# Performance work log

Measured on AMD Instinct MI355X. Metric: run time of the kernel, lower is better.

Reference implementation:

```python
import jax, jax.numpy as jnp
import numpy as np

N = 100000        # num nodes
F_IN = 256        # params['topo_feature']
C = 128           # params['num_edge'] (hidden & GCN channels)
E = 1_600_000     # num edges (avg degree 16)


def setup_inputs() -> dict:
    key = jax.random.key(0)
    k = jax.random.split(key, 6)
    x = jax.random.normal(k[0], (N, F_IN), dtype=jnp.float32)
    edge_index = jax.random.randint(k[1], (2, E), 0, N, dtype=jnp.int32)
    # fc1: Linear(F_IN, C)
    W1 = jax.random.normal(k[2], (C, F_IN), dtype=jnp.float32) * (1.0 / np.sqrt(F_IN))
    b1 = jnp.zeros((C,), dtype=jnp.float32)
    # GCNConv linear: Linear(C, C, bias=False) weight + separate bias added post-aggregation
    W2 = jax.random.normal(k[3], (C, C), dtype=jnp.float32) * (1.0 / np.sqrt(C))
    b2 = jnp.zeros((C,), dtype=jnp.float32)
    return {"x": x, "edge_index": edge_index, "W1": W1, "b1": b1, "W2": W2, "b2": b2}


def reference(x, edge_index, W1, b1, W2, b2):
    # fc1 + relu
    h = jax.nn.relu(x @ W1.T + b1)                       # [N, C]
    # GCNConv: transform, add self-loops, sym-normalize, scatter-add
    z = h @ W2.T                                         # [N, C]
    loop = jnp.arange(N, dtype=edge_index.dtype)
    src = jnp.concatenate([edge_index[0], loop])         # [E+N]
    dst = jnp.concatenate([edge_index[1], loop])         # [E+N]
    deg = jax.ops.segment_sum(jnp.ones_like(dst, jnp.float32), dst, num_segments=N)
    dinv = jnp.where(deg > 0, jax.lax.rsqrt(jnp.maximum(deg, 1.0)), 0.0)
    norm = (dinv[src] * dinv[dst])[:, None]              # [E+N, 1]
    out = jax.ops.segment_sum(z[src] * norm, dst, num_segments=N) + b2
    return out
```

## Files before the change

### kernel.cpp

```cpp
#include <hip/hip_runtime.h>

typedef unsigned short ushort;
typedef __bf16 bf16x8 __attribute__((ext_vector_type(8)));
typedef float f32x4 __attribute__((ext_vector_type(4)));

#define F_IN 256
#define CCH  128
#define BSH  7
#define BNODES 128
#define NBUCK 1024
#define CHUNK 8192

#define LDA 40
#define LDH 136

__device__ __forceinline__ ushort f2bf(float f) {
    union { float f; unsigned i; } u; u.f = f;
    unsigned r = u.i + 0x7fffu + ((u.i >> 16) & 1u);
    return (ushort)(r >> 16);
}
__device__ __forceinline__ float2 bf2f2(unsigned u) {
    union { unsigned i; float f; } lo, hi;
    lo.i = u << 16;
    hi.i = u & 0xffff0000u;
    return make_float2(lo.f, hi.f);
}

__global__ __launch_bounds__(256)
void hist_cvt(const int* __restrict__ dst, int* __restrict__ hist2D, int E, int nchunks,
              const float* __restrict__ W1, const float* __restrict__ W2,
              ushort* __restrict__ w1b, ushort* __restrict__ w2b)
{
    const int blk = blockIdx.x, t = threadIdx.x;
    if (blk >= nchunks) {
        int i = (blk - nchunks) * 256 + t;
        if (i < CCH * F_IN) w1b[i] = f2bf(W1[i]);
        else {
            int j = i - CCH * F_IN;
            if (j < CCH * CCH) w2b[j] = f2bf(W2[j]);
        }
        return;
    }
    __shared__ int h[NBUCK];
    for (int i = t; i < NBUCK; i += 256) h[i] = 0;
    __syncthreads();
    int cb = blk * CHUNK, ce = min(cb + CHUNK, E);
    for (int e = cb + t; e < ce; e += 256)
        atomicAdd(&h[dst[e] >> BSH], 1);
    __syncthreads();
    for (int i = t; i < NBUCK; i += 256)
        hist2D[blk * NBUCK + i] = h[i];
}

__global__ __launch_bounds__(1024)
void scan2d(const int* __restrict__ hist2D, int* __restrict__ pref2D,
            int* __restrict__ base, int nchunks)
{
    __shared__ int s[NBUCK];
    const int t = threadIdx.x;
    int run = 0;
#pragma unroll 4
    for (int c = 0; c < nchunks; c++) {
        int v = hist2D[c * NBUCK + t];
        pref2D[c * NBUCK + t] = run;
        run += v;
    }
    s[t] = run;
    __syncthreads();
    for (int off = 1; off < NBUCK; off <<= 1) {
        int x = (t >= off) ? s[t - off] : 0;
        __syncthreads();
        s[t] += x;
        __syncthreads();
    }
    base[t] = s[t] - run;
    if (t == NBUCK - 1) base[NBUCK] = s[t];
}

__global__ __launch_bounds__(256)
void partition_kernel(const int* __restrict__ src, const int* __restrict__ dst,
                      const int* __restrict__ hist2D, const int* __restrict__ pref2D,
                      const int* __restrict__ base, unsigned* __restrict__ pairs, int E)
{
    __shared__ int lbase[NBUCK];
    __shared__ int lcur[NBUCK];
    __shared__ int rb2[NBUCK];
    __shared__ int ssum[256];
    __shared__ unsigned sp[CHUNK];
    __shared__ ushort  sb[CHUNK];
    const int t = threadIdx.x, blk = blockIdx.x;

    int4 cv = *(const int4*)&hist2D[blk * NBUCK + 4 * t];
    int tsum = cv.x + cv.y + cv.z + cv.w;
    ssum[t] = tsum;
    __syncthreads();
    for (int off = 1; off < 256; off <<= 1) {
        int x = (t >= off) ? ssum[t - off] : 0;
        __syncthreads();
        ssum[t] += x;
        __syncthreads();
    }
    int texcl = ssum[t] - tsum;
    lbase[4 * t]     = texcl;
    lbase[4 * t + 1] = texcl + cv.x;
    lbase[4 * t + 2] = texcl + cv.x + cv.y;
    lbase[4 * t + 3] = texcl + cv.x + cv.y + cv.z;
    lcur[4 * t]     = lbase[4 * t];
    lcur[4 * t + 1] = lbase[4 * t + 1];
    lcur[4 * t + 2] = lbase[4 * t + 2];
    lcur[4 * t + 3] = lbase[4 * t + 3];
    for (int i = t; i < NBUCK; i += 256)
        rb2[i] = base[i] + pref2D[blk * NBUCK + i];
    __syncthreads();

    const int cb = blk * CHUNK, ce = min(cb + CHUNK, E);
    for (int e = cb + t; e < ce; e += 256) {
        int d = dst[e];
        int b = d >> BSH;
        unsigned packed = ((unsigned)src[e] << BSH) | (unsigned)(d & (BNODES - 1));
        int p = atomicAdd(&lcur[b], 1);
        sp[p] = packed;
        sb[p] = (ushort)b;
    }
    __syncthreads();
    const int cnt = ce - cb;
    for (int i = t; i < cnt; i += 256) {
        int b = sb[i];
        pairs[rb2[b] + (i - lbase[b])] = sp[i];
    }
}

__global__ __launch_bounds__(256)
void bucket_csr(const unsigned* __restrict__ pairs, const int* __restrict__ base,
                int* __restrict__ row_start, float* __restrict__ dinv,
                unsigned* __restrict__ csr, int N, int E)
{
    __shared__ int deg[BNODES];
    __shared__ int s[BNODES];
    __shared__ int cur[BNODES];
    const int b = blockIdx.x, t = threadIdx.x;
    if (t < BNODES) deg[t] = 0;
    __syncthreads();
    const int rb = base[b], re = base[b + 1];
    for (int e = rb + t; e < re; e += 256)
        atomicAdd(&deg[pairs[e] & (BNODES - 1)], 1);
    __syncthreads();
    int v = (t < BNODES) ? deg[t] : 0;
    if (t < BNODES) s[t] = v;
    __syncthreads();
    for (int off = 1; off < BNODES; off <<= 1) {
        int x = (t >= off && t < BNODES) ? s[t - off] : 0;
        __syncthreads();
        if (t < BNODES) s[t] += x;
        __syncthreads();
    }
    const int n0 = b << BSH;
    if (t < BNODES) {
        int excl = s[t] - v;
        cur[t] = excl;
        if (n0 + t < N) {
            row_start[n0 + t] = rb + excl;
            dinv[n0 + t] = rsqrtf((float)v + 1.0f);
        }
    }
    if (b == gridDim.x - 1 && t == 0) row_start[N] = E;
    __syncthreads();
    for (int e = rb + t; e < re; e += 256) {
        unsigned p = pairs[e];
        int l = p & (BNODES - 1);
        int slot = atomicAdd(&cur[l], 1);
        csr[rb + slot] = p >> BSH;
    }
}

__global__ __launch_bounds__(256)
void gemm_fused(const float* __restrict__ X, const ushort* __restrict__ W1b,
                const ushort* __restrict__ W2b, const float* __restrict__ b1,
                const float* __restrict__ dinv, ushort* __restrict__ Zq, int M)
{
    __shared__ ushort As[128 * LDA];
    __shared__ ushort Bs[128 * LDA];
    __shared__ ushort Ht[128 * LDH];
    const int tid = threadIdx.x;
    const int wave = tid >> 6, lane = tid & 63;
    const int wm = (wave & 1) * 64, wn = (wave >> 1) * 64;
    const int lr = lane & 15, lq = lane >> 4;
    const int m0 = blockIdx.x * 128;

    f32x4 acc[4][4] = {};
    for (int k0 = 0; k0 < F_IN; k0 += 32) {
#pragma unroll
        for (int it = 0; it < 2; it++) {
            int flat = tid + it * 256;
            int row = flat >> 2, kq = (flat & 3) * 8;
            float4 a0 = make_float4(0.f, 0.f, 0.f, 0.f);
            float4 a1 = make_float4(0.f, 0.f, 0.f, 0.f);
            if (m0 + row < M) {
                a0 = *(const float4*)&X[(long)(m0 + row) * F_IN + k0 + kq];
                a1 = *(const float4*)&X[(long)(m0 + row) * F_IN + k0 + kq + 4];
            }
            ushort u[8] = { f2bf(a0.x), f2bf(a0.y), f2bf(a0.z), f2bf(a0.w),
                            f2bf(a1.x), f2bf(a1.y), f2bf(a1.z), f2bf(a1.w) };
            *(uint4*)&As[row * LDA + kq] = *(uint4*)u;
        }
#pragma unroll
        for (int it = 0; it < 2; it++) {
            int flat = tid + it * 256;
            int row = flat >> 2, kq = (flat & 3) * 8;
            *(uint4*)&Bs[row * LDA + kq] = *(const uint4*)&W1b[(long)row * F_IN + k0 + kq];
        }
        __syncthreads();
        bf16x8 af[4], bfr[4];
#pragma unroll
        for (int t4 = 0; t4 < 4; t4++) {
            af[t4]  = *(bf16x8*)&As[(wm + t4 * 16 + lr) * LDA + lq * 8];
            bfr[t4] = *(bf16x8*)&Bs[(wn + t4 * 16 + lr) * LDA + lq * 8];
        }
#pragma unroll
        for (int i = 0; i < 4; i++)
#pragma unroll
            for (int j = 0; j < 4; j++)
                acc[i][j] = __builtin_amdgcn_mfma_f32_16x16x32_bf16(af[i], bfr[j], acc[i][j], 0, 0, 0);
        __syncthreads();
    }
    {
        float bv[4];
#pragma unroll
        for (int j = 0; j < 4; j++) bv[j] = b1[wn + j * 16 + lr];
#pragma unroll
        for (int i = 0; i < 4; i++)
#pragma unroll
            for (int r = 0; r < 4; r++) {
                int row = wm + i * 16 + lq * 4 + r;
#pragma unroll
                for (int j = 0; j < 4; j++)
                    Ht[row * LDH + wn + j * 16 + lr] = f2bf(fmaxf(acc[i][j][r] + bv[j], 0.f));
            }
    }
    __syncthreads();

    f32x4 acc2[4][4] = {};
    for (int k0 = 0; k0 < CCH; k0 += 32) {
#pragma unroll
        for (int it = 0; it < 2; it++) {
            int flat = tid + it * 256;
            int row = flat >> 2, kq = (flat & 3) * 8;
            *(uint4*)&Bs[row * LDA + kq] = *(const uint4*)&W2b[(long)row * CCH + k0 + kq];
        }
        __syncthreads();
        bf16x8 af[4], bfr[4];
#pragma unroll
        for (int t4 = 0; t4 < 4; t4++) {
            af[t4]  = *(bf16x8*)&Ht[(wm + t4 * 16 + lr) * LDH + k0 + lq * 8];
            bfr[t4] = *(bf16x8*)&Bs[(wn + t4 * 16 + lr) * LDA + lq * 8];
        }
#pragma unroll
        for (int i = 0; i < 4; i++)
#pragma unroll
            for (int j = 0; j < 4; j++)
                acc2[i][j] = __builtin_amdgcn_mfma_f32_16x16x32_bf16(af[i], bfr[j], acc2[i][j], 0, 0, 0);
        __syncthreads();
    }
#pragma unroll
    for (int i = 0; i < 4; i++)
#pragma unroll
        for (int r = 0; r < 4; r++) {
            int row = wm + i * 16 + lq * 4 + r;
            float di = (m0 + row < M) ? dinv[m0 + row] : 0.f;
#pragma unroll
            for (int j = 0; j < 4; j++)
                Ht[row * LDH + wn + j * 16 + lr] = f2bf(acc2[i][j][r] * di);
        }
    __syncthreads();
    {
        int colq = tid & 15, row0 = tid >> 4;
#pragma unroll
        for (int i = 0; i < 8; i++) {
            int row = row0 + i * 16;
            if (m0 + row < M)
                *(uint4*)&Zq[(long)(m0 + row) * CCH + colq * 8] =
                    *(uint4*)&Ht[row * LDH + colq * 8];
        }
    }
}

__global__ __launch_bounds__(256)
void gather_nodes(const unsigned* __restrict__ zq, const unsigned* __restrict__ csr,
                  const int* __restrict__ row_start, const float* __restrict__ dinv,
                  const float* __restrict__ b2, float* __restrict__ out, int N)
{
    const int node = blockIdx.x * 4 + (threadIdx.x >> 6);
    const int lane = threadIdx.x & 63;
    if (node >= N) return;

    float2 zs = bf2f2(zq[(long)node * 64 + lane]);
    float acc0 = zs.x, acc1 = zs.y;

    const int rs = row_start[node];
    const int re = row_start[node + 1];
    int j = rs;
    for (; j + 8 <= re; j += 8) {
        unsigned sI[8], zv[8];
#pragma unroll
        for (int q = 0; q < 8; q++) sI[q] = csr[j + q];
#pragma unroll
        for (int q = 0; q < 8; q++) zv[q] = zq[(long)sI[q] * 64 + lane];
#pragma unroll
        for (int q = 0; q < 8; q++) { float2 f = bf2f2(zv[q]); acc0 += f.x; acc1 += f.y; }
    }
    for (; j < re; j++) {
        float2 f = bf2f2(zq[(long)csr[j] * 64 + lane]);
        acc0 += f.x; acc1 += f.y;
    }

    float di = dinv[node];
    float2 o;
    o.x = b2[lane * 2 + 0] + di * acc0;
    o.y = b2[lane * 2 + 1] + di * acc1;
    *(float2*)&out[(long)node * CCH + lane * 2] = o;
}

extern "C" void kernel_launch(void* const* d_in, const int* in_sizes, int n_in,
                              void* d_out, int out_size, void* d_ws, size_t ws_size,
                              hipStream_t stream)
{
    const float* x  = (const float*)d_in[0];
    const int*   ei = (const int*)d_in[1];
    const float* W1 = (const float*)d_in[2];
    const float* b1 = (const float*)d_in[3];
    const float* W2 = (const float*)d_in[4];
    const float* b2 = (const float*)d_in[5];
    float* out = (float*)d_out;

    const int N = in_sizes[0] / F_IN;
    const int E = in_sizes[1] / 2;
    const int* src = ei;
    const int* dst = ei + E;

    const int nchunks = (E + CHUNK - 1) / CHUNK;
    const int nbuck   = (N + BNODES - 1) / BNODES;
    const int ngrid   = (N + 127) / 128;
    const int ncvt    = (CCH * F_IN + CCH * CCH + 255) / 256;

    char* ws = (char*)d_ws;
    ushort* zq    = (ushort*)ws;   ws += (size_t)N * CCH * 2;
    ushort* w1b   = (ushort*)ws;   ws += (size_t)CCH * F_IN * 2;
    ushort* w2b   = (ushort*)ws;   ws += (size_t)CCH * CCH * 2;
    unsigned* prs = (unsigned*)ws; ws += (size_t)E * 4;
    unsigned* csr = (unsigned*)ws; ws += (size_t)E * 4;
    int* rstart   = (int*)ws;      ws += ((size_t)N + 1) * 4;
    float* dinv   = (float*)ws;    ws += (size_t)N * 4;
    int* hist2D   = (int*)ws;      ws += (size_t)nchunks * NBUCK * 4;
    int* pref2D   = (int*)ws;      ws += (size_t)nchunks * NBUCK * 4;
    int* gbase    = (int*)ws;      ws += (NBUCK + 1) * 4;

    hist_cvt<<<nchunks + ncvt, 256, 0, stream>>>(dst, hist2D, E, nchunks, W1, W2, w1b, w2b);
    scan2d<<<1, 1024, 0, stream>>>(hist2D, pref2D, gbase, nchunks);
    partition_kernel<<<nchunks, 256, 0, stream>>>(src, dst, hist2D, pref2D, gbase, prs, E);
    bucket_csr<<<nbuck, 256, 0, stream>>>(prs, gbase, rstart, dinv, csr, N, E);

    gemm_fused<<<ngrid, 256, 0, stream>>>(x, w1b, w2b, b1, dinv, zq, N);

    gather_nodes<<<(N + 3) / 4, 256, 0, stream>>>((const unsigned*)zq, csr, rstart, dinv, b2, out, N);
}
```

Measured before the change: 338.3 us.

## Parallelize bucket scan, shrink partition chunks, and double-buffer GEMM loads

The single-block 2D histogram scan becomes a wave-per-bucket shuffle scan over a transposed histogram, and the global bucket base is recomputed inside every partition block. Chunk size drops to 2048 edges so the histogram and partition kernels launch more blocks with less shared memory each. The fused GEMM now prefetches the next K-slice of X and the weights into registers, double-buffers its shared tiles to drop one barrier per iteration, and sets an occupancy hint of 3 blocks. In exchange there are four times as many chunks to scan, extra histogram writes, and a redundant base scan in each partition block.

```diff
diff --git a/kernel.cpp b/kernel.cpp
--- a/kernel.cpp
+++ b/kernel.cpp
@@ -9,7 +9,7 @@
 #define BSH  7
 #define BNODES 128
 #define NBUCK 1024
-#define CHUNK 8192
+#define CHUNK 2048
 
 #define LDA 40
 #define LDH 136
@@ -27,7 +27,8 @@
 }
 
 __global__ __launch_bounds__(256)
-void hist_cvt(const int* __restrict__ dst, int* __restrict__ hist2D, int E, int nchunks,
+void hist_cvt(const int* __restrict__ dst, int* __restrict__ histC, int* __restrict__ histT,
+              int E, int nchunks, int ncp,
               const float* __restrict__ W1, const float* __restrict__ W2,
               ushort* __restrict__ w1b, ushort* __restrict__ w2b)
 {
@@ -48,49 +49,51 @@
     for (int e = cb + t; e < ce; e += 256)
         atomicAdd(&h[dst[e] >> BSH], 1);
     __syncthreads();
-    for (int i = t; i < NBUCK; i += 256)
-        hist2D[blk * NBUCK + i] = h[i];
-}
-
-__global__ __launch_bounds__(1024)
-void scan2d(const int* __restrict__ hist2D, int* __restrict__ pref2D,
-            int* __restrict__ base, int nchunks)
-{
-    __shared__ int s[NBUCK];
-    const int t = threadIdx.x;
-    int run = 0;
-#pragma unroll 4
-    for (int c = 0; c < nchunks; c++) {
-        int v = hist2D[c * NBUCK + t];
-        pref2D[c * NBUCK + t] = run;
-        run += v;
-    }
-    s[t] = run;
-    __syncthreads();
-    for (int off = 1; off < NBUCK; off <<= 1) {
-        int x = (t >= off) ? s[t - off] : 0;
-        __syncthreads();
-        s[t] += x;
-        __syncthreads();
-    }
-    base[t] = s[t] - run;
-    if (t == NBUCK - 1) base[NBUCK] = s[t];
+    for (int i = t; i < NBUCK; i += 256) {
+        int v = h[i];
+        histC[blk * NBUCK + i] = v;
+        histT[i * ncp + blk]   = v;
+    }
+}
+
+__global__ __launch_bounds__(256)
+void scan_buckets(const int* __restrict__ histT, int* __restrict__ prefT,
+                  int* __restrict__ btot, int nchunks, int ncp)
+{
+    const int b = blockIdx.x * 4 + (threadIdx.x >> 6);
+    const int lane = threadIdx.x & 63;
+    int carry = 0;
+    for (int c = 0; c < nchunks; c += 64) {
+        int idx = c + lane;
+        int v = (idx < nchunks) ? histT[b * ncp + idx] : 0;
+        int inc = v;
+#pragma unroll
+        for (int off = 1; off < 64; off <<= 1) {
+            int x = __shfl_up(inc, off, 64);
+            if (lane >= off) inc += x;
+        }
+        if (idx < nchunks) prefT[b * ncp + idx] = carry + inc - v;
+        carry += __shfl(inc, 63, 64);
+    }
+    if (lane == 0) btot[b] = carry;
 }
 
 __global__ __launch_bounds__(256)
 void partition_kernel(const int* __restrict__ src, const int* __restrict__ dst,
-                      const int* __restrict__ hist2D, const int* __restrict__ pref2D,
-                      const int* __restrict__ base, unsigned* __restrict__ pairs, int E)
+                      const int* __restrict__ histC, const int* __restrict__ prefT,
+                      const int* __restrict__ btot, int* __restrict__ gbase,
+                      unsigned* __restrict__ pairs, int E, int ncp)
 {
     __shared__ int lbase[NBUCK];
     __shared__ int lcur[NBUCK];
     __shared__ int rb2[NBUCK];
+    __shared__ int base_s[NBUCK];
     __shared__ int ssum[256];
     __shared__ unsigned sp[CHUNK];
     __shared__ ushort  sb[CHUNK];
     const int t = threadIdx.x, blk = blockIdx.x;
 
-    int4 cv = *(const int4*)&hist2D[blk * NBUCK + 4 * t];
+    int4 cv = *(const int4*)&histC[blk * NBUCK + 4 * t];
     int tsum = cv.x + cv.y + cv.z + cv.w;
     ssum[t] = tsum;
     __syncthreads();
@@ -109,8 +112,30 @@
     lcur[4 * t + 1] = lbase[4 * t + 1];
     lcur[4 * t + 2] = lbase[4 * t + 2];
     lcur[4 * t + 3] = lbase[4 * t + 3];
+    __syncthreads();
+
+    int4 bt = *(const int4*)&btot[4 * t];
+    int bsum = bt.x + bt.y + bt.z + bt.w;
+    ssum[t] = bsum;
+    __syncthreads();
+    for (int off = 1; off < 256; off <<= 1) {
+        int x = (t >= off) ? ssum[t - off] : 0;
+        __syncthreads();
+        ssum[t] += x;
+        __syncthreads();
+    }
+    int bexcl = ssum[t] - bsum;
+    base_s[4 * t]     = bexcl;
+    base_s[4 * t + 1] = bexcl + bt.x;
+    base_s[4 * t + 2] = bexcl + bt.x + bt.y;
+    base_s[4 * t + 3] = bexcl + bt.x + bt.y + bt.z;
+    if (blk == 0) {
+        *(int4*)&gbase[4 * t] = *(int4*)&base_s[4 * t];
+        if (t == 255) gbase[NBUCK] = ssum[255];
+    }
+    __syncthreads();
     for (int i = t; i < NBUCK; i += 256)
-        rb2[i] = base[i] + pref2D[blk * NBUCK + i];
+        rb2[i] = base_s[i] + prefT[i * ncp + blk];
     __syncthreads();
 
     const int cb = blk * CHUNK, ce = min(cb + CHUNK, E);
@@ -173,43 +198,65 @@
     }
 }
 
-__global__ __launch_bounds__(256)
+__global__ __launch_bounds__(256, 3)
 void gemm_fused(const float* __restrict__ X, const ushort* __restrict__ W1b,
                 const ushort* __restrict__ W2b, const float* __restrict__ b1,
                 const float* __restrict__ dinv, ushort* __restrict__ Zq, int M)
 {
-    __shared__ ushort As[128 * LDA];
-    __shared__ ushort Bs[128 * LDA];
-    __shared__ ushort Ht[128 * LDH];
+    __shared__ ushort smem[25600];
+    ushort* Ht  = smem;
+    ushort* BsB = smem + 20480;
     const int tid = threadIdx.x;
     const int wave = tid >> 6, lane = tid & 63;
     const int wm = (wave & 1) * 64, wn = (wave >> 1) * 64;
     const int lr = lane & 15, lq = lane >> 4;
     const int m0 = blockIdx.x * 128;
 
+    const int ldr  = tid >> 2;
+    const int ldkq = (tid & 3) * 8;
+
     f32x4 acc[4][4] = {};
+    float4 ar[2][2];
+    uint4  br[2];
+    {
+#pragma unroll
+        for (int it = 0; it < 2; it++) {
+            int row = ldr + it * 64;
+            ar[it][0] = make_float4(0.f, 0.f, 0.f, 0.f);
+            ar[it][1] = make_float4(0.f, 0.f, 0.f, 0.f);
+            if (m0 + row < M) {
+                ar[it][0] = *(const float4*)&X[(long)(m0 + row) * F_IN + ldkq];
+                ar[it][1] = *(const float4*)&X[(long)(m0 + row) * F_IN + ldkq + 4];
+            }
+            br[it] = *(const uint4*)&W1b[(long)row * F_IN + ldkq];
+        }
+    }
     for (int k0 = 0; k0 < F_IN; k0 += 32) {
+        ushort* As = smem + (k0 & 32) * 320;
+        ushort* Bs = As + 5120;
 #pragma unroll
         for (int it = 0; it < 2; it++) {
-            int flat = tid + it * 256;
-            int row = flat >> 2, kq = (flat & 3) * 8;
-            float4 a0 = make_float4(0.f, 0.f, 0.f, 0.f);
-            float4 a1 = make_float4(0.f, 0.f, 0.f, 0.f);
-            if (m0 + row < M) {
-                a0 = *(const float4*)&X[(long)(m0 + row) * F_IN + k0 + kq];
-                a1 = *(const float4*)&X[(long)(m0 + row) * F_IN + k0 + kq + 4];
+            int row = ldr + it * 64;
+            ushort u[8] = { f2bf(ar[it][0].x), f2bf(ar[it][0].y), f2bf(ar[it][0].z), f2bf(ar[it][0].w),
+                            f2bf(ar[it][1].x), f2bf(ar[it][1].y), f2bf(ar[it][1].z), f2bf(ar[it][1].w) };
+            *(uint4*)&As[row * LDA + ldkq] = *(uint4*)u;
+            *(uint4*)&Bs[row * LDA + ldkq] = br[it];
+        }
+        __syncthreads();
+        if (k0 + 32 < F_IN) {
+            int kn = k0 + 32;
+#pragma unroll
+            for (int it = 0; it < 2; it++) {
+                int row = ldr + it * 64;
+                ar[it][0] = make_float4(0.f, 0.f, 0.f, 0.f);
+                ar[it][1] = make_float4(0.f, 0.f, 0.f, 0.f);
+                if (m0 + row < M) {
+                    ar[it][0] = *(const float4*)&X[(long)(m0 + row) * F_IN + kn + ldkq];
+                    ar[it][1] = *(const float4*)&X[(long)(m0 + row) * F_IN + kn + ldkq + 4];
+                }
+                br[it] = *(const uint4*)&W1b[(long)row * F_IN + kn + ldkq];
             }
-            ushort u[8] = { f2bf(a0.x), f2bf(a0.y), f2bf(a0.z), f2bf(a0.w),
-                            f2bf(a1.x), f2bf(a1.y), f2bf(a1.z), f2bf(a1.w) };
-            *(uint4*)&As[row * LDA + kq] = *(uint4*)u;
-        }
-#pragma unroll
-        for (int it = 0; it < 2; it++) {
-            int flat = tid + it * 256;
-            int row = flat >> 2, kq = (flat & 3) * 8;
-            *(uint4*)&Bs[row * LDA + kq] = *(const uint4*)&W1b[(long)row * F_IN + k0 + kq];
-        }
-        __syncthreads();
+        }
         bf16x8 af[4], bfr[4];
 #pragma unroll
         for (int t4 = 0; t4 < 4; t4++) {
@@ -221,8 +268,9 @@
 #pragma unroll
             for (int j = 0; j < 4; j++)
                 acc[i][j] = __builtin_amdgcn_mfma_f32_16x16x32_bf16(af[i], bfr[j], acc[i][j], 0, 0, 0);
-        __syncthreads();
-    }
+    }
+    __syncthreads();
+
     {
         float bv[4];
 #pragma unroll
@@ -240,19 +288,26 @@
     __syncthreads();
 
     f32x4 acc2[4][4] = {};
+    {
+#pragma unroll
+        for (int it = 0; it < 2; it++)
+            br[it] = *(const uint4*)&W2b[(long)(ldr + it * 64) * CCH + ldkq];
+    }
     for (int k0 = 0; k0 < CCH; k0 += 32) {
 #pragma unroll
-        for (int it = 0; it < 2; it++) {
-            int flat = tid + it * 256;
-            int row = flat >> 2, kq = (flat & 3) * 8;
-            *(uint4*)&Bs[row * LDA + kq] = *(const uint4*)&W2b[(long)row * CCH + k0 + kq];
-        }
-        __syncthreads();
+        for (int it = 0; it < 2; it++)
+            *(uint4*)&BsB[(ldr + it * 64) * LDA + ldkq] = br[it];
+        __syncthreads();
+        if (k0 + 32 < CCH) {
+#pragma unroll
+            for (int it = 0; it < 2; it++)
+                br[it] = *(const uint4*)&W2b[(long)(ldr + it * 64) * CCH + k0 + 32 + ldkq];
+        }
         bf16x8 af[4], bfr[4];
 #pragma unroll
         for (int t4 = 0; t4 < 4; t4++) {
             af[t4]  = *(bf16x8*)&Ht[(wm + t4 * 16 + lr) * LDH + k0 + lq * 8];
-            bfr[t4] = *(bf16x8*)&Bs[(wn + t4 * 16 + lr) * LDA + lq * 8];
+            bfr[t4] = *(bf16x8*)&BsB[(wn + t4 * 16 + lr) * LDA + lq * 8];
         }
 #pragma unroll
         for (int i = 0; i < 4; i++)
@@ -261,6 +316,7 @@
                 acc2[i][j] = __builtin_amdgcn_mfma_f32_16x16x32_bf16(af[i], bfr[j], acc2[i][j], 0, 0, 0);
         __syncthreads();
     }
+
 #pragma unroll
     for (int i = 0; i < 4; i++)
 #pragma unroll
@@ -338,6 +394,7 @@
     const int* dst = ei + E;
 
     const int nchunks = (E + CHUNK - 1) / CHUNK;
+    const int ncp     = (nchunks + 63) & ~63;
     const int nbuck   = (N + BNODES - 1) / BNODES;
     const int ngrid   = (N + 127) / 128;
     const int ncvt    = (CCH * F_IN + CCH * CCH + 255) / 256;
@@ -350,13 +407,15 @@
     unsigned* csr = (unsigned*)ws; ws += (size_t)E * 4;
     int* rstart   = (int*)ws;      ws += ((size_t)N + 1) * 4;
     float* dinv   = (float*)ws;    ws += (size_t)N * 4;
-    int* hist2D   = (int*)ws;      ws += (size_t)nchunks * NBUCK * 4;
-    int* pref2D   = (int*)ws;      ws += (size_t)nchunks * NBUCK * 4;
+    int* histC    = (int*)ws;      ws += (size_t)nchunks * NBUCK * 4;
+    int* histT    = (int*)ws;      ws += (size_t)NBUCK * ncp * 4;
+    int* prefT    = (int*)ws;      ws += (size_t)NBUCK * ncp * 4;
+    int* btot     = (int*)ws;      ws += NBUCK * 4;
     int* gbase    = (int*)ws;      ws += (NBUCK + 1) * 4;
 
-    hist_cvt<<<nchunks + ncvt, 256, 0, stream>>>(dst, hist2D, E, nchunks, W1, W2, w1b, w2b);
-    scan2d<<<1, 1024, 0, stream>>>(hist2D, pref2D, gbase, nchunks);
-    partition_kernel<<<nchunks, 256, 0, stream>>>(src, dst, hist2D, pref2D, gbase, prs, E);
+    hist_cvt<<<nchunks + ncvt, 256, 0, stream>>>(dst, histC, histT, E, nchunks, ncp, W1, W2, w1b, w2b);
+    scan_buckets<<<NBUCK / 4, 256, 0, stream>>>(histT, prefT, btot, nchunks, ncp);
+    partition_kernel<<<nchunks, 256, 0, stream>>>(src, dst, histC, prefT, btot, gbase, prs, E, ncp);
     bucket_csr<<<nbuck, 256, 0, stream>>>(prs, gbase, rstart, dinv, csr, N, E);
 
     gemm_fused<<<ngrid, 256, 0, stream>>>(x, w1b, w2b, b1, dinv, zq, N);
```

Result: no change. 341.9 us (+1.1%).
